# Kernel tuning notes

Hardware: AMD Instinct MI355X
Metric: run time of the kernel (lower is better)

Reference implementation:

```python
import jax, jax.numpy as jnp
import numpy as np

B, N, C, H = 2, 2048, 1024, 16
D = C // H  # head_dim = 64


def setup_inputs() -> dict:
    key = jax.random.key(0)
    ks = jax.random.split(key, 10)
    s = 0.02
    return {
        "x": jax.random.normal(ks[0], (B, N, C), dtype=jnp.float32),
        "gauge_theta": jax.random.normal(ks[1], (C,), dtype=jnp.float32),
        "Wg": jax.random.normal(ks[2], (C, C), dtype=jnp.float32) * s,
        "bg": jnp.zeros((C,), dtype=jnp.float32),
        "Wqkv": jax.random.normal(ks[3], (3 * C, C), dtype=jnp.float32) * s,
        "bqkv": jnp.zeros((3 * C,), dtype=jnp.float32),
        "Wproj": jax.random.normal(ks[4], (C, C), dtype=jnp.float32) * s,
        "bproj": jnp.zeros((C,), dtype=jnp.float32),
    }


def reference(x, gauge_theta, Wg, bg, Wqkv, bqkv, Wproj, bproj):
    # gauge-equivariant mixing: x = x + 0.1 * (Linear(x) * theta)
    x_gauge = (jnp.einsum('bnc,oc->bno', x, Wg) + bg) * gauge_theta  # [B,N,C]
    xg = x + 0.1 * x_gauge
    # fused qkv projection -> [B,N,3,H,D] -> q,k,v [B,H,N,D]
    qkv = (jnp.einsum('bnc,oc->bno', xg, Wqkv) + bqkv).reshape(B, N, 3, H, D)
    qkv = jnp.transpose(qkv, (2, 0, 3, 1, 4))
    q, k, v = qkv[0], qkv[1], qkv[2]
    scale = 1.0 / jnp.sqrt(jnp.float32(D))
    attn = jnp.einsum('bhnd,bhmd->bhnm', q, k) * scale  # explicit [B,H,N,N]
    attn = jax.nn.softmax(attn, axis=-1)  # eval mode: no noise, no dropout
    out = jnp.einsum('bhnm,bhmd->bhnd', attn, v)  # [B,H,N,D]
    out = jnp.transpose(out, (0, 2, 1, 3)).reshape(B, N, C)
    return jnp.einsum('bnc,oc->bno', out, Wproj) + bproj
```

## Files before the change

### kernel.cpp

```cpp
#include <hip/hip_runtime.h>
#include <stdint.h>

typedef __bf16 bf16x8 __attribute__((ext_vector_type(8)));
typedef __bf16 bf16x2 __attribute__((ext_vector_type(2)));
typedef float  f32x4  __attribute__((ext_vector_type(4)));
typedef unsigned int u32x4 __attribute__((ext_vector_type(4)));
typedef unsigned short u16;

__device__ __forceinline__ u16 f2bf(float f) {
    return __builtin_bit_cast(u16, (__bf16)f);
}

__device__ __forceinline__ unsigned pk_bf16(float a, float b) {
    bf16x2 r; r[0] = (__bf16)a; r[1] = (__bf16)b;
    return __builtin_bit_cast(unsigned, r);
}

__device__ __forceinline__ bf16x8 ld_frag(const u16* p) {
    u32x4 u = *(const u32x4*)p;
    return __builtin_bit_cast(bf16x8, u);
}

__device__ __forceinline__ void gload16(const u16* g, u16* l) {
    __builtin_amdgcn_global_load_lds(
        (__attribute__((address_space(1))) void*)g,
        (__attribute__((address_space(3))) void*)l,
        16, 0, 0);
}

#define ATT_CSC 0.18033688011112042f

__global__ __launch_bounds__(256) void cvt_all(
    const float* __restrict__ x, const float* __restrict__ wg,
    const float* __restrict__ wqkv, const float* __restrict__ wproj,
    u16* __restrict__ xo, u16* __restrict__ wgo,
    u16* __restrict__ wqkvo, u16* __restrict__ wprojo)
{
    int i = blockIdx.x * 256 + threadIdx.x;
    const float4* in; uint2* out; int off;
    if (i < 1048576)      { in = (const float4*)x;     out = (uint2*)xo;     off = i; }
    else if (i < 1310720) { in = (const float4*)wg;    out = (uint2*)wgo;    off = i - 1048576; }
    else if (i < 2097152) { in = (const float4*)wqkv;  out = (uint2*)wqkvo;  off = i - 1310720; }
    else                  { in = (const float4*)wproj; out = (uint2*)wprojo; off = i - 2097152; }
    float4 v = in[off];
    uint2 o; o.x = pk_bf16(v.x, v.y); o.y = pk_bf16(v.z, v.w);
    out[off] = o;
}

__global__ __launch_bounds__(512, 6) void gemm_bt(
    const u16* __restrict__ A,
    const u16* __restrict__ W,
    const float* __restrict__ bias,
    u16* __restrict__ qo, u16* __restrict__ ko, u16* __restrict__ vTo)
{
    __shared__ alignas(16) u16 As[128 * 64];
    __shared__ alignas(16) u16 Bs[128 * 64];
    const int tid  = threadIdx.x;
    const int wave = tid >> 6, lane = tid & 63;
    const int lquad = lane >> 4, lcol = lane & 15;
    const int wr = (wave >> 2) * 64, wc = (wave & 3) * 32;
    const int rowb = blockIdx.x * 128, colb = blockIdx.y * 128;
    const int srow8 = lane >> 3;
    const int swc = (((lane & 7) ^ srow8) * 8);
    const int rs0 = ((0 * 4 + lquad) ^ (lcol & 7)) * 8;
    const int rs1 = ((1 * 4 + lquad) ^ (lcol & 7)) * 8;

    const u16* gA = A + (size_t)(rowb + wave * 8 + srow8) * 1024 + swc;
    const u16* gB = W + (size_t)(colb + wave * 8 + srow8) * 1024 + swc;
    u16* dA = As + wave * 512;
    u16* dB = Bs + wave * 512;

    f32x4 zero4 = {0.f, 0.f, 0.f, 0.f};
    f32x4 acc[4][2];
#pragma unroll
    for (int i = 0; i < 4; i++)
#pragma unroll
        for (int j = 0; j < 2; j++) acc[i][j] = zero4;

    for (int k0 = 0; k0 < 1024; k0 += 64) {
        __syncthreads();
        gload16(gA + k0, dA);
        gload16(gA + (size_t)64 * 1024 + k0, dA + 64 * 64);
        gload16(gB + k0, dB);
        gload16(gB + (size_t)64 * 1024 + k0, dB + 64 * 64);
        __syncthreads();
#pragma unroll
        for (int db = 0; db < 2; db++) {
            const int rsw = db ? rs1 : rs0;
            bf16x8 af[4], bfr[2];
#pragma unroll
            for (int t = 0; t < 4; t++) af[t]  = ld_frag(As + (wr + t * 16 + lcol) * 64 + rsw);
#pragma unroll
            for (int t = 0; t < 2; t++) bfr[t] = ld_frag(Bs + (wc + t * 16 + lcol) * 64 + rsw);
#pragma unroll
            for (int i = 0; i < 4; i++)
#pragma unroll
                for (int j = 0; j < 2; j++)
                    acc[i][j] = __builtin_amdgcn_mfma_f32_16x16x32_bf16(af[i], bfr[j], acc[i][j], 0, 0, 0);
        }
    }

#pragma unroll
    for (int i = 0; i < 4; i++) {
#pragma unroll
        for (int j = 0; j < 2; j++) {
            int gcol = colb + wc + j * 16 + lcol;
            float bsv = bias[gcol];
            int grow0 = rowb + wr + i * 16 + lquad * 4;
            int three = gcol >> 10, rem = gcol & 1023;
            int h = rem >> 6, d = rem & 63;
            int b = grow0 >> 11, nn = grow0 & 2047;
            int bh = b * 16 + h;
            if (three == 2) {
                ushort4 o;
                o.x = f2bf(acc[i][j][0] + bsv);
                o.y = f2bf(acc[i][j][1] + bsv);
                o.z = f2bf(acc[i][j][2] + bsv);
                o.w = f2bf(acc[i][j][3] + bsv);
                *(ushort4*)(vTo + ((size_t)bh * 64 + d) * 2048 + nn) = o;
            } else if (three == 0) {
#pragma unroll
                for (int r = 0; r < 4; r++)
                    qo[((size_t)bh * 2048 + nn + r) * 64 + d] = f2bf((acc[i][j][r] + bsv) * ATT_CSC);
            } else {
#pragma unroll
                for (int r = 0; r < 4; r++)
                    ko[((size_t)bh * 2048 + nn + r) * 64 + d] = f2bf(acc[i][j][r] + bsv);
            }
        }
    }
}

__global__ __launch_bounds__(512, 4) void gemm64(
    int mode,
    const u16* __restrict__ A,
    const u16* __restrict__ W,
    const float* __restrict__ bias,
    const float* __restrict__ xres,
    const float* __restrict__ theta,
    u16* __restrict__ out_bf,
    float* __restrict__ out_f)
{
    __shared__ alignas(16) u16 As[64 * 64];
    __shared__ alignas(16) u16 Bs[128 * 64];
    const int tid  = threadIdx.x;
    const int wave = tid >> 6, lane = tid & 63;
    const int lquad = lane >> 4, lcol = lane & 15;
    const int wr = (wave & 1) * 32, wc = (wave >> 1) * 32;
    const int rowb = blockIdx.x * 64, colb = blockIdx.y * 128;
    const int srow8 = lane >> 3;
    const int swc = (((lane & 7) ^ srow8) * 8);
    const int rs0 = ((0 * 4 + lquad) ^ (lcol & 7)) * 8;
    const int rs1 = ((1 * 4 + lquad) ^ (lcol & 7)) * 8;

    const u16* gA = A + (size_t)(rowb + wave * 8 + srow8) * 1024 + swc;
    const u16* gB = W + (size_t)(colb + wave * 8 + srow8) * 1024 + swc;
    u16* dA = As + wave * 512;
    u16* dB = Bs + wave * 512;

    f32x4 zero4 = {0.f, 0.f, 0.f, 0.f};
    f32x4 acc[2][2];
#pragma unroll
    for (int i = 0; i < 2; i++)
#pragma unroll
        for (int j = 0; j < 2; j++) acc[i][j] = zero4;

    for (int k0 = 0; k0 < 1024; k0 += 64) {
        __syncthreads();
        gload16(gA + k0, dA);
        gload16(gB + k0, dB);
        gload16(gB + (size_t)64 * 1024 + k0, dB + 64 * 64);
        __syncthreads();
#pragma unroll
        for (int db = 0; db < 2; db++) {
            const int rsw = db ? rs1 : rs0;
            bf16x8 af[2], bfr[2];
#pragma unroll
            for (int t = 0; t < 2; t++) af[t]  = ld_frag(As + (wr + t * 16 + lcol) * 64 + rsw);
#pragma unroll
            for (int t = 0; t < 2; t++) bfr[t] = ld_frag(Bs + (wc + t * 16 + lcol) * 64 + rsw);
#pragma unroll
            for (int i = 0; i < 2; i++)
#pragma unroll
                for (int j = 0; j < 2; j++)
                    acc[i][j] = __builtin_amdgcn_mfma_f32_16x16x32_bf16(af[i], bfr[j], acc[i][j], 0, 0, 0);
        }
    }

#pragma unroll
    for (int i = 0; i < 2; i++) {
#pragma unroll
        for (int j = 0; j < 2; j++) {
            int gcol = colb + wc + j * 16 + lcol;
            float bsv = bias[gcol];
            int grow0 = rowb + wr + i * 16 + lquad * 4;
            if (mode == 0) {
#pragma unroll
                for (int r = 0; r < 4; r++) {
                    size_t idx = (size_t)(grow0 + r) * 1024 + gcol;
                    float val = acc[i][j][r] + bsv;
                    out_bf[idx] = f2bf(xres[idx] + 0.1f * (val * theta[gcol]));
                }
            } else {
#pragma unroll
                for (int r = 0; r < 4; r++)
                    out_f[(size_t)(grow0 + r) * 1024 + gcol] = acc[i][j][r] + bsv;
            }
        }
    }
}

__global__ __launch_bounds__(512, 4) void attn_kernel(
    const u16* __restrict__ q,
    const u16* __restrict__ k,
    const u16* __restrict__ vT,
    u16* __restrict__ attnout)
{
    __shared__ alignas(16) u16 smem[32768];

    const int tid  = threadIdx.x;
    const int wave = tid >> 6, lane = tid & 63;
    const int g = wave >> 2, wq = wave & 3;
    const int lquad = lane >> 4, lcol = lane & 15;
    const int bh   = blockIdx.y;
    const int row0 = blockIdx.x * 128 + wq * 32;
    const int rsw  = (lquad ^ (lcol & 3)) * 8;

    u16* KsG = smem + g * 8192;
    u16* VsG = smem + 16384 + g * 8192;

    bf16x8 qf[2][2];
#pragma unroll
    for (int qh = 0; qh < 2; qh++)
#pragma unroll
        for (int db = 0; db < 2; db++)
            qf[qh][db] = ld_frag(q + ((size_t)bh * 2048 + row0 + qh * 16 + lcol) * 64 + db * 32 + lquad * 8);

    const int sb = wq & 1;
    const int srow = lane >> 2;
    const int swc  = (((lane & 3) ^ (srow & 3)) * 8);
    const u16* gK = k  + ((size_t)bh * 2048 + srow) * 64 + sb * 32 + swc;
    const u16* gV = vT + ((size_t)bh * 64 + srow) * 2048 + sb * 32 + swc;

    auto stage = [&](int it, int buf) {
        int j0 = g * 1024 + it * 64;
        if ((wq & 2) == 0) {
            u16* ldst = KsG + buf * 4096 + sb * 2048;
#pragma unroll
            for (int i = 0; i < 4; i++)
                gload16(gK + (size_t)(j0 + i * 16) * 64, ldst + i * 16 * 32);
        } else {
            u16* ldst = VsG + buf * 4096 + sb * 2048;
#pragma unroll
            for (int i = 0; i < 4; i++)
                gload16(gV + (size_t)(i * 16) * 2048 + j0, ldst + i * 16 * 32);
        }
    };

    f32x4 zero4 = {0.f, 0.f, 0.f, 0.f};
    f32x4 lacc[2] = {zero4, zero4};
    f32x4 oacc[2][4];
#pragma unroll
    for (int qh = 0; qh < 2; qh++)
#pragma unroll
        for (int dt = 0; dt < 4; dt++) oacc[qh][dt] = zero4;

    stage(0, 0);
    __syncthreads();

    for (int it = 0; it < 16; ++it) {
        const int buf = it & 1;
        if (it < 15) stage(it + 1, buf ^ 1);

        const u16* Kt = KsG + buf * 4096;
        const u16* Vt = VsG + buf * 4096;

        f32x4 sacc[2][4];
        __builtin_amdgcn_s_setprio(1);
#pragma unroll
        for (int jt = 0; jt < 4; jt++)
#pragma unroll
            for (int db = 0; db < 2; db++) {
                bf16x8 kf = ld_frag(Kt + db * 2048 + (jt * 16 + lcol) * 32 + rsw);
#pragma unroll
                for (int qh = 0; qh < 2; qh++)
                    sacc[qh][jt] = __builtin_amdgcn_mfma_f32_16x16x32_bf16(
                        kf, qf[qh][db], db == 0 ? zero4 : sacc[qh][jt], 0, 0, 0);
            }
        __builtin_amdgcn_s_setprio(0);

        unsigned dpk[2][4][2];
#pragma unroll
        for (int qh = 0; qh < 2; qh++) {
#pragma unroll
            for (int jt = 0; jt < 4; jt++) {
                f32x4 pe;
                pe[0] = __builtin_amdgcn_exp2f(sacc[qh][jt][0]);
                pe[1] = __builtin_amdgcn_exp2f(sacc[qh][jt][1]);
                pe[2] = __builtin_amdgcn_exp2f(sacc[qh][jt][2]);
                pe[3] = __builtin_amdgcn_exp2f(sacc[qh][jt][3]);
                lacc[qh] += pe;
                dpk[qh][jt][0] = pk_bf16(pe[0], pe[1]);
                dpk[qh][jt][1] = pk_bf16(pe[2], pe[3]);
            }
        }

        bf16x8 pf[2][2];
#pragma unroll
        for (int qh = 0; qh < 2; qh++) {
#pragma unroll
            for (int kb = 0; kb < 2; kb++) {
                unsigned Ax = dpk[qh][2 * kb][0],     Ay = dpk[qh][2 * kb][1];
                unsigned Bx = dpk[qh][2 * kb + 1][0], By = dpk[qh][2 * kb + 1][1];
                u32x4 w;
#if __has_builtin(__builtin_amdgcn_permlane32_swap) && __has_builtin(__builtin_amdgcn_permlane16_swap)
                {
                    auto s1 = __builtin_amdgcn_permlane32_swap(Ax, Bx, false, false);
                    auto s2 = __builtin_amdgcn_permlane16_swap(s1[0], s1[1], false, false);
                    w[0] = s2[0]; w[2] = s2[1];
                    auto s3 = __builtin_amdgcn_permlane32_swap(Ay, By, false, false);
                    auto s4 = __builtin_amdgcn_permlane16_swap(s3[0], s3[1], false, false);
                    w[1] = s4[0]; w[3] = s4[1];
                }
#else
                {
                    unsigned x1x = (lquad < 2) ? Bx : Ax;
                    unsigned x1y = (lquad < 2) ? By : Ay;
                    unsigned r1x = __shfl_xor(x1x, 32, 64);
                    unsigned r1y = __shfl_xor(x1y, 32, 64);
                    unsigned x2x = (lquad == 1) ? Ax : (lquad == 2) ? Bx : r1x;
                    unsigned x2y = (lquad == 1) ? Ay : (lquad == 2) ? By : r1y;
                    unsigned r2x = __shfl_xor(x2x, 16, 64);
                    unsigned r2y = __shfl_xor(x2y, 16, 64);
                    w[0] = (lquad == 0) ? Ax : (lquad == 2) ? r1x : r2x;
                    w[1] = (lquad == 0) ? Ay : (lquad == 2) ? r1y : r2y;
                    w[2] = (lquad == 1) ? r1x : (lquad == 3) ? Bx : r2x;
                    w[3] = (lquad == 1) ? r1y : (lquad == 3) ? By : r2y;
                }
#endif
                pf[qh][kb] = __builtin_bit_cast(bf16x8, w);
            }
        }

        __builtin_amdgcn_s_setprio(1);
#pragma unroll
        for (int dt = 0; dt < 4; dt++)
#pragma unroll
            for (int kb = 0; kb < 2; kb++) {
                bf16x8 vf = ld_frag(Vt + kb * 2048 + (dt * 16 + lcol) * 32 + rsw);
#pragma unroll
                for (int qh = 0; qh < 2; qh++)
                    oacc[qh][dt] = __builtin_amdgcn_mfma_f32_16x16x32_bf16(vf, pf[qh][kb], oacc[qh][dt], 0, 0, 0);
            }
        __builtin_amdgcn_s_setprio(0);

        __syncthreads();
    }

    float* scr = (float*)smem;
    const int slot = wq * 64 + lane;
    if (g == 1) {
#pragma unroll
        for (int qh = 0; qh < 2; qh++) {
#pragma unroll
            for (int dt = 0; dt < 4; dt++)
                *(f32x4*)&scr[slot * 44 + qh * 16 + dt * 4] = oacc[qh][dt];
            *(f32x4*)&scr[slot * 44 + 32 + qh * 4] = lacc[qh];
        }
    }
    __syncthreads();
    if (g == 1) return;

#pragma unroll
    for (int qh = 0; qh < 2; qh++) {
#pragma unroll
        for (int dt = 0; dt < 4; dt++)
            oacc[qh][dt] += *(const f32x4*)&scr[slot * 44 + qh * 16 + dt * 4];
        lacc[qh] += *(const f32x4*)&scr[slot * 44 + 32 + qh * 4];
    }

    const int b = bh >> 4, h = bh & 15;
#pragma unroll
    for (int qh = 0; qh < 2; qh++) {
        float l = (lacc[qh][0] + lacc[qh][1]) + (lacc[qh][2] + lacc[qh][3]);
        l += __shfl_xor(l, 16, 64);
        l += __shfl_xor(l, 32, 64);
        float inv = 1.0f / l;
        const int n = row0 + qh * 16 + lcol;
        size_t base = ((size_t)b * 2048 + n) * 1024 + h * 64;
#pragma unroll
        for (int dt = 0; dt < 4; dt++) {
            uint2 o;
            o.x = pk_bf16(oacc[qh][dt][0] * inv, oacc[qh][dt][1] * inv);
            o.y = pk_bf16(oacc[qh][dt][2] * inv, oacc[qh][dt][3] * inv);
            *(uint2*)(attnout + base + dt * 16 + lquad * 4) = o;
        }
    }
}

extern "C" void kernel_launch(void* const* d_in, const int* in_sizes, int n_in,
                              void* d_out, int out_size, void* d_ws, size_t ws_size,
                              hipStream_t stream) {
    const float* x     = (const float*)d_in[0];
    const float* theta = (const float*)d_in[1];
    const float* Wg    = (const float*)d_in[2];
    const float* bg    = (const float*)d_in[3];
    const float* Wqkv  = (const float*)d_in[4];
    const float* bqkv  = (const float*)d_in[5];
    const float* Wproj = (const float*)d_in[6];
    const float* bproj = (const float*)d_in[7];
    float* out = (float*)d_out;

    unsigned char* ws = (unsigned char*)d_ws;
    const size_t MB = 1ull << 20;
    u16* x_bf     = (u16*)(ws + 0);
    u16* Wg_bf    = (u16*)(ws + 8 * MB);
    u16* Wqkv_bf  = (u16*)(ws + 10 * MB);
    u16* Wproj_bf = (u16*)(ws + 16 * MB);
    u16* xg_bf    = (u16*)(ws + 18 * MB);
    u16* q_bf     = (u16*)(ws + 26 * MB);
    u16* k_bf     = (u16*)(ws + 34 * MB);
    u16* vT_bf    = (u16*)(ws + 42 * MB);
    u16* ao_bf    = (u16*)(ws + 50 * MB);

    dim3 blk(256);
    cvt_all<<<9216, blk, 0, stream>>>(x, Wg, Wqkv, Wproj,
                                      x_bf, Wg_bf, Wqkv_bf, Wproj_bf);

    gemm64<<<dim3(64, 8), dim3(512), 0, stream>>>(0, x_bf, Wg_bf, bg,
                                                  x, theta, xg_bf, nullptr);
    gemm_bt<<<dim3(32, 24), dim3(512), 0, stream>>>(xg_bf, Wqkv_bf, bqkv,
                                                    q_bf, k_bf, vT_bf);
    attn_kernel<<<dim3(16, 32), dim3(512), 0, stream>>>(q_bf, k_bf, vT_bf, ao_bf);
    gemm64<<<dim3(64, 8), dim3(512), 0, stream>>>(2, ao_bf, Wproj_bf, bproj,
                                                  nullptr, nullptr, nullptr, out);
}
```

Before: 191.2 us.

## Load K/V fragments directly from global and compute row sums via MFMA

Removes the double-buffered LDS staging of K and V tiles and per-iteration block barriers, having each wave read K and V^T fragments straight from global memory (relying on L1/L2 caching). Also replaces the per-lane exp accumulation plus cross-lane shuffles with an MFMA against a ones vector to produce softmax denominators. This cuts LDS footprint and sync overhead but increases redundant global/L2 traffic since the 8 waves no longer share staged tiles, and the row sum now uses bf16-rounded probabilities.

```diff
diff --git a/kernel.cpp b/kernel.cpp
--- a/kernel.cpp
+++ b/kernel.cpp
@@ -216,7 +216,7 @@
     const u16* __restrict__ vT,
     u16* __restrict__ attnout)
 {
-    __shared__ alignas(16) u16 smem[32768];
+    __shared__ alignas(16) float scr[256 * 36];
 
     const int tid  = threadIdx.x;
     const int wave = tid >> 6, lane = tid & 63;
@@ -224,10 +224,6 @@
     const int lquad = lane >> 4, lcol = lane & 15;
     const int bh   = blockIdx.y;
     const int row0 = blockIdx.x * 128 + wq * 32;
-    const int rsw  = (lquad ^ (lcol & 3)) * 8;
-
-    u16* KsG = smem + g * 8192;
-    u16* VsG = smem + 16384 + g * 8192;
 
     bf16x8 qf[2][2];
 #pragma unroll
@@ -236,44 +232,23 @@
         for (int db = 0; db < 2; db++)
             qf[qh][db] = ld_frag(q + ((size_t)bh * 2048 + row0 + qh * 16 + lcol) * 64 + db * 32 + lquad * 8);
 
-    const int sb = wq & 1;
-    const int srow = lane >> 2;
-    const int swc  = (((lane & 3) ^ (srow & 3)) * 8);
-    const u16* gK = k  + ((size_t)bh * 2048 + srow) * 64 + sb * 32 + swc;
-    const u16* gV = vT + ((size_t)bh * 64 + srow) * 2048 + sb * 32 + swc;
-
-    auto stage = [&](int it, int buf) {
-        int j0 = g * 1024 + it * 64;
-        if ((wq & 2) == 0) {
-            u16* ldst = KsG + buf * 4096 + sb * 2048;
-#pragma unroll
-            for (int i = 0; i < 4; i++)
-                gload16(gK + (size_t)(j0 + i * 16) * 64, ldst + i * 16 * 32);
-        } else {
-            u16* ldst = VsG + buf * 4096 + sb * 2048;
-#pragma unroll
-            for (int i = 0; i < 4; i++)
-                gload16(gV + (size_t)(i * 16) * 2048 + j0, ldst + i * 16 * 32);
-        }
-    };
+    const u16* kbase = k  + (size_t)bh * 2048 * 64 + lquad * 8;
+    const u16* vbase = vT + (size_t)bh * 64 * 2048 + lquad * 8;
+
+    bf16x8 ones;
+#pragma unroll
+    for (int e = 0; e < 8; e++) ones[e] = (__bf16)1.0f;
 
     f32x4 zero4 = {0.f, 0.f, 0.f, 0.f};
-    f32x4 lacc[2] = {zero4, zero4};
+    f32x4 lsum[2] = {zero4, zero4};
     f32x4 oacc[2][4];
 #pragma unroll
     for (int qh = 0; qh < 2; qh++)
 #pragma unroll
         for (int dt = 0; dt < 4; dt++) oacc[qh][dt] = zero4;
 
-    stage(0, 0);
-    __syncthreads();
-
     for (int it = 0; it < 16; ++it) {
-        const int buf = it & 1;
-        if (it < 15) stage(it + 1, buf ^ 1);
-
-        const u16* Kt = KsG + buf * 4096;
-        const u16* Vt = VsG + buf * 4096;
+        const int j0 = g * 1024 + it * 64;
 
         f32x4 sacc[2][4];
         __builtin_amdgcn_s_setprio(1);
@@ -281,7 +256,7 @@
         for (int jt = 0; jt < 4; jt++)
 #pragma unroll
             for (int db = 0; db < 2; db++) {
-                bf16x8 kf = ld_frag(Kt + db * 2048 + (jt * 16 + lcol) * 32 + rsw);
+                bf16x8 kf = ld_frag(kbase + (size_t)(j0 + jt * 16 + lcol) * 64 + db * 32);
 #pragma unroll
                 for (int qh = 0; qh < 2; qh++)
                     sacc[qh][jt] = __builtin_amdgcn_mfma_f32_16x16x32_bf16(
@@ -299,7 +274,6 @@
                 pe[1] = __builtin_amdgcn_exp2f(sacc[qh][jt][1]);
                 pe[2] = __builtin_amdgcn_exp2f(sacc[qh][jt][2]);
                 pe[3] = __builtin_amdgcn_exp2f(sacc[qh][jt][3]);
-                lacc[qh] += pe;
                 dpk[qh][jt][0] = pk_bf16(pe[0], pe[1]);
                 dpk[qh][jt][1] = pk_bf16(pe[2], pe[3]);
             }
@@ -347,25 +321,27 @@
         for (int dt = 0; dt < 4; dt++)
 #pragma unroll
             for (int kb = 0; kb < 2; kb++) {
-                bf16x8 vf = ld_frag(Vt + kb * 2048 + (dt * 16 + lcol) * 32 + rsw);
+                bf16x8 vf = ld_frag(vbase + (size_t)(dt * 16 + lcol) * 2048 + j0 + kb * 32);
 #pragma unroll
                 for (int qh = 0; qh < 2; qh++)
                     oacc[qh][dt] = __builtin_amdgcn_mfma_f32_16x16x32_bf16(vf, pf[qh][kb], oacc[qh][dt], 0, 0, 0);
             }
+#pragma unroll
+        for (int qh = 0; qh < 2; qh++)
+#pragma unroll
+            for (int kb = 0; kb < 2; kb++)
+                lsum[qh] = __builtin_amdgcn_mfma_f32_16x16x32_bf16(ones, pf[qh][kb], lsum[qh], 0, 0, 0);
         __builtin_amdgcn_s_setprio(0);
-
-        __syncthreads();
-    }
-
-    float* scr = (float*)smem;
+    }
+
     const int slot = wq * 64 + lane;
     if (g == 1) {
 #pragma unroll
         for (int qh = 0; qh < 2; qh++) {
 #pragma unroll
             for (int dt = 0; dt < 4; dt++)
-                *(f32x4*)&scr[slot * 44 + qh * 16 + dt * 4] = oacc[qh][dt];
-            *(f32x4*)&scr[slot * 44 + 32 + qh * 4] = lacc[qh];
+                *(f32x4*)&scr[slot * 36 + qh * 16 + dt * 4] = oacc[qh][dt];
+            scr[slot * 36 + 32 + qh] = lsum[qh][0];
         }
     }
     __syncthreads();
@@ -375,17 +351,14 @@
     for (int qh = 0; qh < 2; qh++) {
 #pragma unroll
         for (int dt = 0; dt < 4; dt++)
-            oacc[qh][dt] += *(const f32x4*)&scr[slot * 44 + qh * 16 + dt * 4];
-        lacc[qh] += *(const f32x4*)&scr[slot * 44 + 32 + qh * 4];
+            oacc[qh][dt] += *(const f32x4*)&scr[slot * 36 + qh * 16 + dt * 4];
+        lsum[qh][0] += scr[slot * 36 + 32 + qh];
     }
 
     const int b = bh >> 4, h = bh & 15;
 #pragma unroll
     for (int qh = 0; qh < 2; qh++) {
-        float l = (lacc[qh][0] + lacc[qh][1]) + (lacc[qh][2] + lacc[qh][3]);
-        l += __shfl_xor(l, 16, 64);
-        l += __shfl_xor(l, 32, 64);
-        float inv = 1.0f / l;
+        float inv = 1.0f / lsum[qh][0];
         const int n = row0 + qh * 16 + lcol;
         size_t base = ((size_t)b * 2048 + n) * 1024 + h * 64;
 #pragma unroll
```

Result: slower. 279.0 us (+45.9%).

## Double-buffer LDS tiles in the QKV and 64-row GEMMs with prefetch

Applied to the files above, without the earlier changes.

Both GEMM kernels now keep two LDS buffers and prefetch the next K-slice with global_load_lds while MFMAs run on the current one, using one barrier per iteration instead of two. gemm_bt shrinks its K-step to 32 so the doubled buffers fit in the same LDS footprint, which needs a new swizzle, and s_setprio raises wave priority around the MFMA blocks. The goal is to hide global load latency behind compute. The cost is more LDS in gemm64, which can lower occupancy, and twice as many loop iterations in gemm_bt.

```diff
diff --git a/kernel.cpp b/kernel.cpp
--- a/kernel.cpp
+++ b/kernel.cpp
@@ -53,22 +53,18 @@
     const float* __restrict__ bias,
     u16* __restrict__ qo, u16* __restrict__ ko, u16* __restrict__ vTo)
 {
-    __shared__ alignas(16) u16 As[128 * 64];
-    __shared__ alignas(16) u16 Bs[128 * 64];
+    __shared__ alignas(16) u16 As[2][128 * 32];
+    __shared__ alignas(16) u16 Bs[2][128 * 32];
     const int tid  = threadIdx.x;
     const int wave = tid >> 6, lane = tid & 63;
     const int lquad = lane >> 4, lcol = lane & 15;
     const int wr = (wave >> 2) * 64, wc = (wave & 3) * 32;
     const int rowb = blockIdx.x * 128, colb = blockIdx.y * 128;
-    const int srow8 = lane >> 3;
-    const int swc = (((lane & 7) ^ srow8) * 8);
-    const int rs0 = ((0 * 4 + lquad) ^ (lcol & 7)) * 8;
-    const int rs1 = ((1 * 4 + lquad) ^ (lcol & 7)) * 8;
-
-    const u16* gA = A + (size_t)(rowb + wave * 8 + srow8) * 1024 + swc;
-    const u16* gB = W + (size_t)(colb + wave * 8 + srow8) * 1024 + swc;
-    u16* dA = As + wave * 512;
-    u16* dB = Bs + wave * 512;
+    const int swc = (((lane & 3) ^ ((lane >> 2) & 3)) * 8);
+    const int rsw = (lquad ^ (lcol & 3)) * 8;
+
+    const u16* gA = A + (size_t)(rowb + wave * 16 + (lane >> 2)) * 1024 + swc;
+    const u16* gB = W + (size_t)(colb + wave * 16 + (lane >> 2)) * 1024 + swc;
 
     f32x4 zero4 = {0.f, 0.f, 0.f, 0.f};
     f32x4 acc[4][2];
@@ -77,27 +73,32 @@
 #pragma unroll
         for (int j = 0; j < 2; j++) acc[i][j] = zero4;
 
-    for (int k0 = 0; k0 < 1024; k0 += 64) {
+    auto stage = [&](int k0, int buf) {
+        gload16(gA + k0, As[buf] + wave * 512);
+        gload16(gB + k0, Bs[buf] + wave * 512);
+    };
+
+    stage(0, 0);
+    __syncthreads();
+
+    for (int it = 0; it < 32; ++it) {
+        const int buf = it & 1;
+        if (it < 31) stage((it + 1) * 32, buf ^ 1);
+
+        bf16x8 af[4], bfr[2];
+#pragma unroll
+        for (int t = 0; t < 4; t++) af[t]  = ld_frag(As[buf] + (wr + t * 16 + lcol) * 32 + rsw);
+#pragma unroll
+        for (int t = 0; t < 2; t++) bfr[t] = ld_frag(Bs[buf] + (wc + t * 16 + lcol) * 32 + rsw);
+        __builtin_amdgcn_s_setprio(1);
+#pragma unroll
+        for (int i = 0; i < 4; i++)
+#pragma unroll
+            for (int j = 0; j < 2; j++)
+                acc[i][j] = __builtin_amdgcn_mfma_f32_16x16x32_bf16(af[i], bfr[j], acc[i][j], 0, 0, 0);
+        __builtin_amdgcn_s_setprio(0);
+
         __syncthreads();
-        gload16(gA + k0, dA);
-        gload16(gA + (size_t)64 * 1024 + k0, dA + 64 * 64);
-        gload16(gB + k0, dB);
-        gload16(gB + (size_t)64 * 1024 + k0, dB + 64 * 64);
-        __syncthreads();
-#pragma unroll
-        for (int db = 0; db < 2; db++) {
-            const int rsw = db ? rs1 : rs0;
-            bf16x8 af[4], bfr[2];
-#pragma unroll
-            for (int t = 0; t < 4; t++) af[t]  = ld_frag(As + (wr + t * 16 + lcol) * 64 + rsw);
-#pragma unroll
-            for (int t = 0; t < 2; t++) bfr[t] = ld_frag(Bs + (wc + t * 16 + lcol) * 64 + rsw);
-#pragma unroll
-            for (int i = 0; i < 4; i++)
-#pragma unroll
-                for (int j = 0; j < 2; j++)
-                    acc[i][j] = __builtin_amdgcn_mfma_f32_16x16x32_bf16(af[i], bfr[j], acc[i][j], 0, 0, 0);
-        }
     }
 
 #pragma unroll
@@ -141,8 +142,8 @@
     u16* __restrict__ out_bf,
     float* __restrict__ out_f)
 {
-    __shared__ alignas(16) u16 As[64 * 64];
-    __shared__ alignas(16) u16 Bs[128 * 64];
+    __shared__ alignas(16) u16 As[2][64 * 64];
+    __shared__ alignas(16) u16 Bs[2][128 * 64];
     const int tid  = threadIdx.x;
     const int wave = tid >> 6, lane = tid & 63;
     const int lquad = lane >> 4, lcol = lane & 15;
@@ -155,8 +156,6 @@
 
     const u16* gA = A + (size_t)(rowb + wave * 8 + srow8) * 1024 + swc;
     const u16* gB = W + (size_t)(colb + wave * 8 + srow8) * 1024 + swc;
-    u16* dA = As + wave * 512;
-    u16* dB = Bs + wave * 512;
 
     f32x4 zero4 = {0.f, 0.f, 0.f, 0.f};
     f32x4 acc[2][2];
@@ -165,26 +164,37 @@
 #pragma unroll
         for (int j = 0; j < 2; j++) acc[i][j] = zero4;
 
-    for (int k0 = 0; k0 < 1024; k0 += 64) {
-        __syncthreads();
-        gload16(gA + k0, dA);
-        gload16(gB + k0, dB);
-        gload16(gB + (size_t)64 * 1024 + k0, dB + 64 * 64);
-        __syncthreads();
+    auto stage = [&](int k0, int buf) {
+        gload16(gA + k0, As[buf] + wave * 512);
+        gload16(gB + k0, Bs[buf] + wave * 512);
+        gload16(gB + (size_t)64 * 1024 + k0, Bs[buf] + 64 * 64 + wave * 512);
+    };
+
+    stage(0, 0);
+    __syncthreads();
+
+    for (int it = 0; it < 16; ++it) {
+        const int buf = it & 1;
+        if (it < 15) stage((it + 1) * 64, buf ^ 1);
+
 #pragma unroll
         for (int db = 0; db < 2; db++) {
             const int rsw = db ? rs1 : rs0;
             bf16x8 af[2], bfr[2];
 #pragma unroll
-            for (int t = 0; t < 2; t++) af[t]  = ld_frag(As + (wr + t * 16 + lcol) * 64 + rsw);
-#pragma unroll
-            for (int t = 0; t < 2; t++) bfr[t] = ld_frag(Bs + (wc + t * 16 + lcol) * 64 + rsw);
+            for (int t = 0; t < 2; t++) af[t]  = ld_frag(As[buf] + (wr + t * 16 + lcol) * 64 + rsw);
+#pragma unroll
+            for (int t = 0; t < 2; t++) bfr[t] = ld_frag(Bs[buf] + (wc + t * 16 + lcol) * 64 + rsw);
+            __builtin_amdgcn_s_setprio(1);
 #pragma unroll
             for (int i = 0; i < 2; i++)
 #pragma unroll
                 for (int j = 0; j < 2; j++)
                     acc[i][j] = __builtin_amdgcn_mfma_f32_16x16x32_bf16(af[i], bfr[j], acc[i][j], 0, 0, 0);
-        }
+            __builtin_amdgcn_s_setprio(0);
+        }
+
+        __syncthreads();
     }
 
 #pragma unroll
```

New measurement: 201.1 us. +5.1%, slower.

## Fold gauge linear layer into QKV weights instead of applying it to activations

Applied to the files above, without the earlier changes.

Uses linearity to precompute W' = Wqkv + 0.1*Wqkv*diag(theta)*Wg and an adjusted bias, then runs the QKV GEMM directly on x. This replaces a 4096x1024x1024 activation GEMM with a 3072x1024x1024 weight-only GEMM, and the prep kernel gains a transposed, theta-scaled Wg and a bias reduction. Folding in bf16 changes rounding, since the folded weights are rounded to bf16 again, and the weight fold runs on every call.

```diff
diff --git a/kernel.cpp b/kernel.cpp
--- a/kernel.cpp
+++ b/kernel.cpp
@@ -11,6 +11,10 @@
     return __builtin_bit_cast(u16, (__bf16)f);
 }
 
+__device__ __forceinline__ float bf2f(u16 v) {
+    return (float)__builtin_bit_cast(__bf16, v);
+}
+
 __device__ __forceinline__ unsigned pk_bf16(float a, float b) {
     bf16x2 r; r[0] = (__bf16)a; r[1] = (__bf16)b;
     return __builtin_bit_cast(unsigned, r);
@@ -30,21 +34,62 @@
 
 #define ATT_CSC 0.18033688011112042f
 
-__global__ __launch_bounds__(256) void cvt_all(
-    const float* __restrict__ x, const float* __restrict__ wg,
-    const float* __restrict__ wqkv, const float* __restrict__ wproj,
-    u16* __restrict__ xo, u16* __restrict__ wgo,
-    u16* __restrict__ wqkvo, u16* __restrict__ wprojo)
+__global__ __launch_bounds__(256) void prep_all(
+    const float* __restrict__ x, const float* __restrict__ wqkv,
+    const float* __restrict__ wproj, const float* __restrict__ wg,
+    const float* __restrict__ theta, const float* __restrict__ bg,
+    const float* __restrict__ bqkv,
+    u16* __restrict__ xo, u16* __restrict__ wqkvo, u16* __restrict__ wprojo,
+    u16* __restrict__ wgT, float* __restrict__ bvec)
 {
-    int i = blockIdx.x * 256 + threadIdx.x;
-    const float4* in; uint2* out; int off;
-    if (i < 1048576)      { in = (const float4*)x;     out = (uint2*)xo;     off = i; }
-    else if (i < 1310720) { in = (const float4*)wg;    out = (uint2*)wgo;    off = i - 1048576; }
-    else if (i < 2097152) { in = (const float4*)wqkv;  out = (uint2*)wqkvo;  off = i - 1310720; }
-    else                  { in = (const float4*)wproj; out = (uint2*)wprojo; off = i - 2097152; }
-    float4 v = in[off];
-    uint2 o; o.x = pk_bf16(v.x, v.y); o.y = pk_bf16(v.z, v.w);
-    out[off] = o;
+    __shared__ float tile[64][65];
+    const int blk = blockIdx.x, tid = threadIdx.x;
+    if (blk < 8192) {
+        int i = blk * 256 + tid;
+        const float4* in; uint2* out; int off;
+        if (i < 1048576)      { in = (const float4*)x;     out = (uint2*)xo;     off = i; }
+        else if (i < 1835008) { in = (const float4*)wqkv;  out = (uint2*)wqkvo;  off = i - 1048576; }
+        else                  { in = (const float4*)wproj; out = (uint2*)wprojo; off = i - 1835008; }
+        float4 v = in[off];
+        uint2 o; o.x = pk_bf16(v.x, v.y); o.y = pk_bf16(v.z, v.w);
+        out[off] = o;
+    } else if (blk < 8448) {
+        int t = blk - 8192;
+        int m0 = (t >> 4) * 64, c0 = (t & 15) * 64;
+#pragma unroll
+        for (int p = 0; p < 4; p++) {
+            int id = p * 256 + tid;
+            int r = id >> 4, q = id & 15;
+            float4 v = *(const float4*)(wg + (size_t)(m0 + r) * 1024 + c0 + q * 4);
+            tile[r][q * 4 + 0] = v.x; tile[r][q * 4 + 1] = v.y;
+            tile[r][q * 4 + 2] = v.z; tile[r][q * 4 + 3] = v.w;
+        }
+        __syncthreads();
+        int c = tid >> 2, mc = (tid & 3) * 16;
+        u32x4 w0, w1;
+#pragma unroll
+        for (int i = 0; i < 8; i++) {
+            float a = theta[m0 + mc + 2 * i]     * tile[mc + 2 * i][c];
+            float b = theta[m0 + mc + 2 * i + 1] * tile[mc + 2 * i + 1][c];
+            unsigned pk = pk_bf16(a, b);
+            if (i < 4) w0[i] = pk; else w1[i - 4] = pk;
+        }
+        u16* dst = wgT + (size_t)(c0 + c) * 1024 + m0 + mc;
+        *(u32x4*)dst = w0;
+        *(u32x4*)(dst + 8) = w1;
+    } else {
+        const int wave = tid >> 6, lane = tid & 63;
+        const int o = (blk - 8448) * 4 + wave;
+        const float* wr = wqkv + (size_t)o * 1024 + lane * 16;
+        const float* tp = theta + lane * 16;
+        const float* bp = bg + lane * 16;
+        float s = 0.f;
+#pragma unroll
+        for (int i = 0; i < 16; i++) s += wr[i] * tp[i] * bp[i];
+        s += __shfl_xor(s, 1);  s += __shfl_xor(s, 2);  s += __shfl_xor(s, 4);
+        s += __shfl_xor(s, 8);  s += __shfl_xor(s, 16); s += __shfl_xor(s, 32);
+        if (lane == 0) bvec[o] = bqkv[o] + 0.1f * s;
+    }
 }
 
 __global__ __launch_bounds__(512, 6) void gemm_bt(
@@ -136,8 +181,6 @@
     const u16* __restrict__ A,
     const u16* __restrict__ W,
     const float* __restrict__ bias,
-    const float* __restrict__ xres,
-    const float* __restrict__ theta,
     u16* __restrict__ out_bf,
     float* __restrict__ out_f)
 {
@@ -192,16 +235,15 @@
 #pragma unroll
         for (int j = 0; j < 2; j++) {
             int gcol = colb + wc + j * 16 + lcol;
-            float bsv = bias[gcol];
             int grow0 = rowb + wr + i * 16 + lquad * 4;
-            if (mode == 0) {
+            if (mode == 1) {
 #pragma unroll
                 for (int r = 0; r < 4; r++) {
                     size_t idx = (size_t)(grow0 + r) * 1024 + gcol;
-                    float val = acc[i][j][r] + bsv;
-                    out_bf[idx] = f2bf(xres[idx] + 0.1f * (val * theta[gcol]));
+                    out_bf[idx] = f2bf(bf2f(A[idx]) + 0.1f * acc[i][j][r]);
                 }
             } else {
+                float bsv = bias[gcol];
 #pragma unroll
                 for (int r = 0; r < 4; r++)
                     out_f[(size_t)(grow0 + r) * 1024 + gcol] = acc[i][j][r] + bsv;
@@ -414,24 +456,24 @@
     unsigned char* ws = (unsigned char*)d_ws;
     const size_t MB = 1ull << 20;
     u16* x_bf     = (u16*)(ws + 0);
-    u16* Wg_bf    = (u16*)(ws + 8 * MB);
+    u16* WgT_bf   = (u16*)(ws + 8 * MB);
     u16* Wqkv_bf  = (u16*)(ws + 10 * MB);
     u16* Wproj_bf = (u16*)(ws + 16 * MB);
-    u16* xg_bf    = (u16*)(ws + 18 * MB);
+    u16* Wqp_bf   = (u16*)(ws + 18 * MB);
+    float* bvec   = (float*)(ws + 24 * MB);
     u16* q_bf     = (u16*)(ws + 26 * MB);
     u16* k_bf     = (u16*)(ws + 34 * MB);
     u16* vT_bf    = (u16*)(ws + 42 * MB);
     u16* ao_bf    = (u16*)(ws + 50 * MB);
 
-    dim3 blk(256);
-    cvt_all<<<9216, blk, 0, stream>>>(x, Wg, Wqkv, Wproj,
-                                      x_bf, Wg_bf, Wqkv_bf, Wproj_bf);
-
-    gemm64<<<dim3(64, 8), dim3(512), 0, stream>>>(0, x_bf, Wg_bf, bg,
-                                                  x, theta, xg_bf, nullptr);
-    gemm_bt<<<dim3(32, 24), dim3(512), 0, stream>>>(xg_bf, Wqkv_bf, bqkv,
+    prep_all<<<9216, 256, 0, stream>>>(x, Wqkv, Wproj, Wg, theta, bg, bqkv,
+                                       x_bf, Wqkv_bf, Wproj_bf, WgT_bf, bvec);
+
+    gemm64<<<dim3(48, 8), dim3(512), 0, stream>>>(1, Wqkv_bf, WgT_bf, nullptr,
+                                                  Wqp_bf, nullptr);
+    gemm_bt<<<dim3(32, 24), dim3(512), 0, stream>>>(x_bf, Wqp_bf, bvec,
                                                     q_bf, k_bf, vT_bf);
     attn_kernel<<<dim3(16, 32), dim3(512), 0, stream>>>(q_bf, k_bf, vT_bf, ao_bf);
     gemm64<<<dim3(64, 8), dim3(512), 0, stream>>>(2, ao_bf, Wproj_bf, bproj,
-                                                  nullptr, nullptr, nullptr, out);
-}
+                                                  nullptr, out);
+}
```

Result: slower. 202.3 us (+5.8%).
